# Optimization experiments

Measured on AMD Instinct MI355X. Metric: run time of the kernel, lower is better.

Reference implementation:

```python
import jax, jax.numpy as jnp
import numpy as np

N = 4096   # nodes
E = 65536  # edges
D_IN = 64
H = 128
T = 8
B = 8


def setup_inputs() -> dict:
    key = jax.random.key(0)
    ks = jax.random.split(key, 6)
    x = jax.random.normal(ks[0], (B, T, N, D_IN), jnp.float32)
    edge_index = jax.random.randint(ks[1], (2, E), 0, N, dtype=jnp.int32)
    W0 = jax.random.normal(ks[2], (D_IN + H, 4 * H), jnp.float32) * 0.05
    b0 = jax.random.normal(ks[3], (4 * H,), jnp.float32) * 0.05
    W1 = jax.random.normal(ks[4], (H + H, 4 * H), jnp.float32) * 0.05
    b1 = jax.random.normal(ks[5], (4 * H,), jnp.float32) * 0.05
    return {"x": x, "W0": W0, "b0": b0, "W1": W1, "b1": b1, "edge_index": edge_index}


def _gcn_norm(edge_index, n):
    # PyG GCNConv(improved=True): A_hat = A + 2I, deg over incoming edges (col)
    src, dst = edge_index[0], edge_index[1]
    deg = jax.ops.segment_sum(jnp.ones(edge_index.shape[1], jnp.float32), dst, num_segments=n) + 2.0
    dinv = jax.lax.rsqrt(deg)  # deg >= 2 always, safe
    return src, dst, dinv


def _gcn_gates(comb, W, b, src, dst, dinv, n):
    # comb: (b, n, i+h) -> gates: (b, n, 4h)
    xw = jnp.einsum('bnf,fg->bng', comb, W)
    norm_e = dinv[src] * dinv[dst]                      # (E,)
    msgs = xw[:, src, :] * norm_e[None, :, None]        # (b, E, 4h)
    agg = jax.vmap(lambda m: jax.ops.segment_sum(m, dst, num_segments=n))(msgs)
    # self-loop with weight 2: norm = 2 * dinv[i]^2
    agg = agg + (2.0 * dinv * dinv)[None, :, None] * xw + b
    return agg


def reference(x, W0, b0, W1, b1, edge_index):
    src, dst, dinv = _gcn_norm(edge_index, N)

    def run_layer(seq, W, b):
        h_dim = W.shape[1] // 4

        def step(carry, xt):
            h, c = carry
            comb = jnp.concatenate([xt, h], axis=-1)
            gates = _gcn_gates(comb, W, b, src, dst, dinv, N)
            ci, cf, co, cg = jnp.split(gates, 4, axis=-1)
            i = jax.nn.sigmoid(ci)
            f = jax.nn.sigmoid(cf)
            o = jax.nn.sigmoid(co)
            g = jnp.tanh(cg)
            c_next = f * c + i * g
            h_next = o * jnp.tanh(c_next)
            return (h_next, c_next), h_next

        h0 = jnp.zeros((seq.shape[1], N, h_dim), seq.dtype)
        _, hs = jax.lax.scan(step, (h0, h0), seq)
        return hs  # (t, b, n, h)

    seq = jnp.swapaxes(x, 0, 1)  # batch_first -> (t, b, n, d)
    hs0 = run_layer(seq, W0, b0)
    hs1 = run_layer(hs0, W1, b1)
    return jnp.swapaxes(hs1, 0, 1)  # (b, t, n, h) last-layer output sequence
```

## Files before the change

kernel.cpp:

```cpp
#include <hip/hip_runtime.h>
#include <hip/hip_fp16.h>
#include <math.h>

constexpr int N_NODES = 4096;
constexpr int N_EDGES = 65536;
constexpr int D_INF   = 64;
constexpr int H       = 128;
constexpr int T       = 8;
constexpr int B       = 8;
constexpr int M       = B * N_NODES;

typedef __attribute__((ext_vector_type(8))) short bf16x8;
typedef __attribute__((ext_vector_type(4))) float f32x4;
typedef __attribute__((ext_vector_type(8))) _Float16 f16x8;

__device__ inline unsigned short f2bf(float x) {
  unsigned int u = __float_as_uint(x);
  unsigned int r = (u + 0x7fffu + ((u >> 16) & 1u)) >> 16;
  return (unsigned short)r;
}
__device__ inline float bf2f(unsigned short b) {
  return __uint_as_float((unsigned int)b << 16);
}
__device__ __forceinline__ int swz(int s) { return s ^ (((s >> 7) & 7) << 3); }


__global__ void k_count(const int* __restrict__ dst, int* __restrict__ cnt) {
  int e = blockIdx.x * blockDim.x + threadIdx.x;
  if (e < N_EDGES) atomicAdd(&cnt[dst[e]], 1);
}

__global__ void k_dinv(const int* __restrict__ cnt, float* __restrict__ dinv) {
  int n = blockIdx.x * blockDim.x + threadIdx.x;
  if (n < N_NODES) dinv[n] = 1.0f / sqrtf((float)cnt[n] + 2.0f);
}

__global__ void k_scan(const int* __restrict__ cnt, int* __restrict__ rowptr) {
  __shared__ int sums[1024];
  int t = threadIdx.x;
  int v0 = cnt[4*t+0], v1 = cnt[4*t+1], v2 = cnt[4*t+2], v3 = cnt[4*t+3];
  int s0 = v0, s1 = s0 + v1, s2 = s1 + v2, s3 = s2 + v3;
  sums[t] = s3;
  __syncthreads();
  for (int off = 1; off < 1024; off <<= 1) {
    int x = (t >= off) ? sums[t - off] : 0;
    __syncthreads();
    sums[t] += x;
    __syncthreads();
  }
  int base = (t > 0) ? sums[t - 1] : 0;
  if (t == 0) rowptr[0] = 0;
  rowptr[4*t+1] = base + s0;
  rowptr[4*t+2] = base + s1;
  rowptr[4*t+3] = base + s2;
  rowptr[4*t+4] = base + s3;
}

__global__ void k_fill(const int* __restrict__ src, const int* __restrict__ dst,
                       const float* __restrict__ dinv, const int* __restrict__ rowptr,
                       int* __restrict__ fill, int2* __restrict__ eg) {
  int e = blockIdx.x * blockDim.x + threadIdx.x;
  if (e >= N_EDGES) return;
  int s = src[e], d = dst[e];
  int p = rowptr[d] + atomicAdd(&fill[d], 1);
  eg[p] = make_int2(s, __float_as_int(dinv[s] * dinv[d]));
}

__global__ void k_pack(const float* __restrict__ W, unsigned short* __restrict__ Bp,
                       int K) {
  int tid = blockIdx.x * 256 + threadIdx.x;
  if (tid >= K * 64) return;
  int lane = tid & 63;
  int ntg  = (tid >> 6) & 31;
  int kb   = tid >> 11;
  int gate = ntg & 3, fg = ntg >> 2;
  int corig = gate * 128 + fg * 16 + (lane & 15);
  int k0 = kb * 32 + (lane >> 4) * 8;
  long obase = ((long)(kb * 32 + ntg) * 64 + lane) * 8;
  long plane = (long)K * 512;
  #pragma unroll
  for (int j = 0; j < 8; ++j) {
    float v = W[(long)(k0 + j) * 512 + corig];
    unsigned short h = f2bf(v);
    Bp[obase + j]         = h;
    Bp[plane + obase + j] = f2bf(v - bf2f(h));
  }
}

template<int K, bool L0>
__global__ __launch_bounds__(512, 4) void k_fused(
    const int* __restrict__ rowptr, const int2* __restrict__ eg,
    const float* __restrict__ dinv,
    const float* __restrict__ X32,
    const _Float16* __restrict__ PH0,
    const _Float16* __restrict__ PH1,
    const unsigned short* __restrict__ Bp, const float* __restrict__ bias,
    _Float16* __restrict__ hout, float* __restrict__ cbuf,
    float* __restrict__ out2, int t) {
  constexpr int KB = K / 32;
  __shared__ __align__(16) unsigned short At[8 * KB * 64 * 8];
  int tid  = threadIdx.x;
  int lane = tid & 63;
  int w    = tid >> 6;
  int j    = blockIdx.x;
  int b    = j & 7;
  int n0   = (j >> 3) * 64;
  int m0   = b * N_NODES + n0;
  int g    = lane >> 4, l = lane & 15;
  int c4   = l * 4, c8 = l * 8;

  const float*    Ax   = L0 ? (X32 + (long)b * ((long)T * N_NODES * D_INF)) : nullptr;
  const _Float16* Ah_p = L0 ? nullptr : (PH0 + (long)b * N_NODES * H);
  const _Float16* Bh_p = (L0 ? PH0 : PH1) + (long)b * N_NODES * H;
  constexpr int kbB0 = (L0 ? 64 : 128) >> 5;
  int lane2f = 16 * (l & 3);
  int kbB    = kbB0 + (c8 >> 5);
  int kbA16  = c8 >> 5;
  int kbA32  = c4 >> 5;
  int subA32 = (l & 7) >> 1;
  int j0A32  = (l & 1) * 4;

  #pragma unroll
  for (int nd = 0; nd < 2; ++nd) {
    int r  = (w << 3) + (g << 1) + nd;
    int n  = n0 + r;
    int rs = rowptr[n], re = rowptr[n + 1];
    float accA[8] = {0.f,0.f,0.f,0.f,0.f,0.f,0.f,0.f};
    float accB[8] = {0.f,0.f,0.f,0.f,0.f,0.f,0.f,0.f};
    int e = rs;
    for (; e + 3 < re; e += 4) {
      int2 q0 = eg[e], q1 = eg[e + 1], q2 = eg[e + 2], q3 = eg[e + 3];
      float w0 = __int_as_float(q0.y), w1 = __int_as_float(q1.y);
      float w2 = __int_as_float(q2.y), w3 = __int_as_float(q3.y);
      if constexpr (L0) {
        f32x4 a0 = *(const f32x4*)(Ax + (long)q0.x * D_INF + c4);
        f32x4 a1 = *(const f32x4*)(Ax + (long)q1.x * D_INF + c4);
        f32x4 a2 = *(const f32x4*)(Ax + (long)q2.x * D_INF + c4);
        f32x4 a3 = *(const f32x4*)(Ax + (long)q3.x * D_INF + c4);
        #pragma unroll
        for (int q = 0; q < 4; ++q)
          accA[q] += w0 * a0[q] + w1 * a1[q] + w2 * a2[q] + w3 * a3[q];
      } else {
        f16x8 a0 = *(const f16x8*)(Ah_p + (long)q0.x * H + c8);
        f16x8 a1 = *(const f16x8*)(Ah_p + (long)q1.x * H + c8);
        f16x8 a2 = *(const f16x8*)(Ah_p + (long)q2.x * H + c8);
        f16x8 a3 = *(const f16x8*)(Ah_p + (long)q3.x * H + c8);
        #pragma unroll
        for (int q = 0; q < 8; ++q)
          accA[q] += w0 * (float)a0[q] + w1 * (float)a1[q]
                   + w2 * (float)a2[q] + w3 * (float)a3[q];
      }
      f16x8 b0 = *(const f16x8*)(Bh_p + (long)q0.x * H + c8);
      f16x8 b1 = *(const f16x8*)(Bh_p + (long)q1.x * H + c8);
      f16x8 b2 = *(const f16x8*)(Bh_p + (long)q2.x * H + c8);
      f16x8 b3 = *(const f16x8*)(Bh_p + (long)q3.x * H + c8);
      #pragma unroll
      for (int q = 0; q < 8; ++q)
        accB[q] += w0 * (float)b0[q] + w1 * (float)b1[q]
                 + w2 * (float)b2[q] + w3 * (float)b3[q];
    }
    for (; e < re; ++e) {
      int2 q0 = eg[e];
      float w0 = __int_as_float(q0.y);
      if constexpr (L0) {
        f32x4 a0 = *(const f32x4*)(Ax + (long)q0.x * D_INF + c4);
        #pragma unroll
        for (int q = 0; q < 4; ++q) accA[q] += w0 * a0[q];
      } else {
        f16x8 a0 = *(const f16x8*)(Ah_p + (long)q0.x * H + c8);
        #pragma unroll
        for (int q = 0; q < 8; ++q) accA[q] += w0 * (float)a0[q];
      }
      f16x8 b0 = *(const f16x8*)(Bh_p + (long)q0.x * H + c8);
      #pragma unroll
      for (int q = 0; q < 8; ++q) accB[q] += w0 * (float)b0[q];
    }
    float dn = dinv[n];
    float sw = 2.0f * dn * dn;
    if constexpr (L0) {
      f32x4 a = *(const f32x4*)(Ax + (long)n * D_INF + c4);
      #pragma unroll
      for (int q = 0; q < 4; ++q) accA[q] += sw * a[q];
    } else {
      f16x8 a = *(const f16x8*)(Ah_p + (long)n * H + c8);
      #pragma unroll
      for (int q = 0; q < 8; ++q) accA[q] += sw * (float)a[q];
    }
    {
      f16x8 v = *(const f16x8*)(Bh_p + (long)n * H + c8);
      #pragma unroll
      for (int q = 0; q < 8; ++q) accB[q] += sw * (float)v[q];
    }

    int mt    = r >> 4;
    int lane2 = (r & 15) + lane2f;
    {
      bf16x8 hv, lv;
      #pragma unroll
      for (int q = 0; q < 8; ++q) {
        unsigned short hs = f2bf(accB[q]);
        hv[q] = (short)hs;
        lv[q] = (short)f2bf(accB[q] - bf2f(hs));
      }
      *(bf16x8*)(At + swz((((mt)     * KB + kbB) * 64 + lane2) * 8)) = hv;
      *(bf16x8*)(At + swz((((4 + mt) * KB + kbB) * 64 + lane2) * 8)) = lv;
    }
    if constexpr (L0) {
      unsigned long long hv = 0ull, lv = 0ull;
      #pragma unroll
      for (int q = 0; q < 4; ++q) {
        unsigned short hs = f2bf(accA[q]);
        unsigned short ls = f2bf(accA[q] - bf2f(hs));
        hv |= (unsigned long long)hs << (16 * q);
        lv |= (unsigned long long)ls << (16 * q);
      }
      int lA = (r & 15) + 16 * subA32;
      *(unsigned long long*)(At + swz((((mt)     * KB + kbA32) * 64 + lA) * 8 + j0A32)) = hv;
      *(unsigned long long*)(At + swz((((4 + mt) * KB + kbA32) * 64 + lA) * 8 + j0A32)) = lv;
    } else {
      bf16x8 hv, lv;
      #pragma unroll
      for (int q = 0; q < 8; ++q) {
        unsigned short hs = f2bf(accA[q]);
        hv[q] = (short)hs;
        lv[q] = (short)f2bf(accA[q] - bf2f(hs));
      }
      *(bf16x8*)(At + swz((((mt)     * KB + kbA16) * 64 + lane2) * 8)) = hv;
      *(bf16x8*)(At + swz((((4 + mt) * KB + kbA16) * 64 + lane2) * 8)) = lv;
    }
  }
  __syncthreads();

  int l15 = lane & 15, lq = lane >> 4;
  const unsigned short* bb  = Bp + (long)(w * 4) * 512 + lane * 8;
  const unsigned short* blp = bb + (long)K * 512;

  f32x4 acc[4][4];
  #pragma unroll
  for (int mt = 0; mt < 4; ++mt)
    #pragma unroll
    for (int gt = 0; gt < 4; ++gt)
      acc[mt][gt] = (f32x4){0.f, 0.f, 0.f, 0.f};

  __builtin_amdgcn_s_setprio(1);
  #pragma unroll 2
  for (int kb = 0; kb < KB; ++kb) {
    bf16x8 AH_[4], AL_[4];
    #pragma unroll
    for (int mt = 0; mt < 4; ++mt) {
      AH_[mt] = *(const bf16x8*)(At + swz((((mt)     * KB + kb) * 64 + lane) * 8));
      AL_[mt] = *(const bf16x8*)(At + swz((((4 + mt) * KB + kb) * 64 + lane) * 8));
    }
    bf16x8 BH[4], BL[4];
    #pragma unroll
    for (int gt = 0; gt < 4; ++gt) {
      BH[gt] = *(const bf16x8*)(bb  + ((long)kb * 32 + gt) * 512);
      BL[gt] = *(const bf16x8*)(blp + ((long)kb * 32 + gt) * 512);
    }
    #pragma unroll
    for (int gt = 0; gt < 4; ++gt) {
      #pragma unroll
      for (int mt = 0; mt < 4; ++mt) {
        acc[mt][gt] = __builtin_amdgcn_mfma_f32_16x16x32_bf16(AH_[mt], BH[gt], acc[mt][gt], 0, 0, 0);
        acc[mt][gt] = __builtin_amdgcn_mfma_f32_16x16x32_bf16(AL_[mt], BH[gt], acc[mt][gt], 0, 0, 0);
        acc[mt][gt] = __builtin_amdgcn_mfma_f32_16x16x32_bf16(AH_[mt], BL[gt], acc[mt][gt], 0, 0, 0);
      }
    }
  }
  __builtin_amdgcn_s_setprio(0);

  int f = w * 16 + l15;
  float bi = bias[f], bff = bias[128 + f], bo = bias[256 + f], bg = bias[384 + f];
  #pragma unroll
  for (int mt = 0; mt < 4; ++mt) {
    #pragma unroll
    for (int r = 0; r < 4; ++r) {
      int m = m0 + mt * 16 + lq * 4 + r;
      float vi = 1.0f / (1.0f + __expf(-(acc[mt][0][r] + bi)));
      float vf = 1.0f / (1.0f + __expf(-(acc[mt][1][r] + bff)));
      float vo = 1.0f / (1.0f + __expf(-(acc[mt][2][r] + bo)));
      float vg = tanhf(acc[mt][3][r] + bg);
      long idx = (long)m * H + f;
      float cn = vf * cbuf[idx] + vi * vg;
      float hn = vo * tanhf(cn);
      cbuf[idx] = cn;
      hout[idx] = (_Float16)hn;
      if (out2) {
        int bb2 = m >> 12, nn = m & (N_NODES - 1);
        __builtin_nontemporal_store(hn,
            &out2[(((long)bb2 * T + t) * N_NODES + nn) * H + f]);
      }
    }
  }
}


extern "C" void kernel_launch(void* const* d_in, const int* in_sizes, int n_in,
                              void* d_out, int out_size, void* d_ws, size_t ws_size,
                              hipStream_t stream) {
  const float* x  = (const float*)d_in[0];
  const float* W0 = (const float*)d_in[1];
  const float* b0 = (const float*)d_in[2];
  const float* W1 = (const float*)d_in[3];
  const float* b1 = (const float*)d_in[4];
  const int*   ei = (const int*)d_in[5];
  const int* srcp = ei;
  const int* dstp = ei + N_EDGES;
  float* out = (float*)d_out;

  char* p = (char*)d_ws;
  auto alloc = [&](size_t bytes) {
    char* r = p;
    p += (bytes + 255) & ~(size_t)255;
    return r;
  };
  int*   cnt    = (int*)  alloc(N_NODES * 4);
  int*   fill   = (int*)  alloc(N_NODES * 4);
  float* dinv   = (float*)alloc(N_NODES * 4);
  int*   rowptr = (int*)  alloc((N_NODES + 1) * 4);
  int2*  eg     = (int2*) alloc((size_t)N_EDGES * 8);
  float* cc     = (float*)alloc((size_t)2 * M * H * 4);
  _Float16* hh  = (_Float16*)alloc((size_t)4 * M * H * 2);
  unsigned short* Bp0 = (unsigned short*)alloc((size_t)192 * 512 * 2 * 2);
  unsigned short* Bp1 = (unsigned short*)alloc((size_t)256 * 512 * 2 * 2);
  float*    c0  = cc;
  float*    c1  = cc + (size_t)M * H;
  _Float16* h0a = hh;
  _Float16* h0b = hh + (size_t)M * H;
  _Float16* h1a = hh + (size_t)2 * M * H;
  _Float16* h1b = hh + (size_t)3 * M * H;

  hipMemsetAsync(cnt,  0, N_NODES * 4, stream);
  hipMemsetAsync(fill, 0, N_NODES * 4, stream);
  hipMemsetAsync(cc,   0, (size_t)2 * M * H * 4, stream);
  hipMemsetAsync(hh,   0, (size_t)4 * M * H * 2, stream);

  k_count<<<N_EDGES / 256, 256, 0, stream>>>(dstp, cnt);
  k_dinv <<<N_NODES / 256, 256, 0, stream>>>(cnt, dinv);
  k_scan <<<1, 1024, 0, stream>>>(cnt, rowptr);
  k_fill <<<N_EDGES / 256, 256, 0, stream>>>(srcp, dstp, dinv, rowptr, fill, eg);
  k_pack <<<(192 * 64 + 255) / 256, 256, 0, stream>>>(W0, Bp0, 192);
  k_pack <<<(256 * 64 + 255) / 256, 256, 0, stream>>>(W1, Bp1, 256);

  for (int t = 0; t < T; ++t) {
    const _Float16* h0r = (t & 1) ? h0b : h0a;
    _Float16*       h0w = (t & 1) ? h0a : h0b;
    const _Float16* h1r = (t & 1) ? h1b : h1a;
    _Float16*       h1w = (t & 1) ? h1a : h1b;
    k_fused<192, true><<<512, 512, 0, stream>>>(rowptr, eg, dinv,
        x + (size_t)t * N_NODES * D_INF, h0r, nullptr,
        Bp0, b0, h0w, c0, nullptr, t);
    k_fused<256, false><<<512, 512, 0, stream>>>(rowptr, eg, dinv,
        nullptr, h0w, h1r,
        Bp1, b1, h1w, c1, out, t);
  }
}
```

Baseline: 795.9 us.

## Sort nodes by degree and pair light/heavy nodes for balanced gather

Adds a counting sort of nodes by in-degree and remaps each block's rows so every lane group processes one low-degree and one high-degree node. This evens out the per-wave edge-gather loop length, reducing divergence and tail imbalance in the fused aggregation kernel. Output rows are written through an LDS node map, which makes epilogue stores scattered per row and adds a few small preprocessing kernels.

```diff
diff --git a/kernel.cpp b/kernel.cpp
--- a/kernel.cpp
+++ b/kernel.cpp
@@ -64,6 +64,33 @@
   int s = src[e], d = dst[e];
   int p = rowptr[d] + atomicAdd(&fill[d], 1);
   eg[p] = make_int2(s, __float_as_int(dinv[s] * dinv[d]));
+}
+
+__global__ void k_hist(const int* __restrict__ cnt, int* __restrict__ hist) {
+  int n = blockIdx.x * blockDim.x + threadIdx.x;
+  if (n < N_NODES) atomicAdd(&hist[min(cnt[n], 127)], 1);
+}
+
+__global__ void k_hscan(const int* __restrict__ hist, int* __restrict__ hbase) {
+  __shared__ int sh[128];
+  int t = threadIdx.x;
+  sh[t] = hist[t];
+  __syncthreads();
+  for (int off = 1; off < 128; off <<= 1) {
+    int x = (t >= off) ? sh[t - off] : 0;
+    __syncthreads();
+    sh[t] += x;
+    __syncthreads();
+  }
+  hbase[t] = sh[t] - hist[t];
+}
+
+__global__ void k_place(const int* __restrict__ cnt, const int* __restrict__ hbase,
+                        int* __restrict__ filld, int* __restrict__ sorted) {
+  int n = blockIdx.x * blockDim.x + threadIdx.x;
+  if (n >= N_NODES) return;
+  int d = min(cnt[n], 127);
+  sorted[hbase[d] + atomicAdd(&filld[d], 1)] = n;
 }
 
 __global__ void k_pack(const float* __restrict__ W, unsigned short* __restrict__ Bp,
@@ -90,7 +117,7 @@
 template<int K, bool L0>
 __global__ __launch_bounds__(512, 4) void k_fused(
     const int* __restrict__ rowptr, const int2* __restrict__ eg,
-    const float* __restrict__ dinv,
+    const float* __restrict__ dinv, const int* __restrict__ sorted,
     const float* __restrict__ X32,
     const _Float16* __restrict__ PH0,
     const _Float16* __restrict__ PH1,
@@ -99,13 +126,13 @@
     float* __restrict__ out2, int t) {
   constexpr int KB = K / 32;
   __shared__ __align__(16) unsigned short At[8 * KB * 64 * 8];
+  __shared__ int nodeLDS[64];
   int tid  = threadIdx.x;
   int lane = tid & 63;
   int w    = tid >> 6;
   int j    = blockIdx.x;
   int b    = j & 7;
-  int n0   = (j >> 3) * 64;
-  int m0   = b * N_NODES + n0;
+  int jj   = j >> 3;
   int g    = lane >> 4, l = lane & 15;
   int c4   = l * 4, c8 = l * 8;
 
@@ -123,7 +150,9 @@
   #pragma unroll
   for (int nd = 0; nd < 2; ++nd) {
     int r  = (w << 3) + (g << 1) + nd;
-    int n  = n0 + r;
+    int pairIdx = jj * 32 + (r >> 1);
+    int n  = (r & 1) ? sorted[N_NODES - 1 - pairIdx] : sorted[pairIdx];
+    if (l == 0) nodeLDS[r] = n;
     int rs = rowptr[n], re = rowptr[n + 1];
     float accA[8] = {0.f,0.f,0.f,0.f,0.f,0.f,0.f,0.f};
     float accB[8] = {0.f,0.f,0.f,0.f,0.f,0.f,0.f,0.f};
@@ -275,20 +304,20 @@
   for (int mt = 0; mt < 4; ++mt) {
     #pragma unroll
     for (int r = 0; r < 4; ++r) {
-      int m = m0 + mt * 16 + lq * 4 + r;
+      int rt = mt * 16 + lq * 4 + r;
+      int n2 = nodeLDS[rt];
       float vi = 1.0f / (1.0f + __expf(-(acc[mt][0][r] + bi)));
       float vf = 1.0f / (1.0f + __expf(-(acc[mt][1][r] + bff)));
       float vo = 1.0f / (1.0f + __expf(-(acc[mt][2][r] + bo)));
       float vg = tanhf(acc[mt][3][r] + bg);
-      long idx = (long)m * H + f;
+      long idx = ((long)b * N_NODES + n2) * H + f;
       float cn = vf * cbuf[idx] + vi * vg;
       float hn = vo * tanhf(cn);
       cbuf[idx] = cn;
       hout[idx] = (_Float16)hn;
       if (out2) {
-        int bb2 = m >> 12, nn = m & (N_NODES - 1);
         __builtin_nontemporal_store(hn,
-            &out2[(((long)bb2 * T + t) * N_NODES + nn) * H + f]);
+            &out2[(((long)b * T + t) * N_NODES + n2) * H + f]);
       }
     }
   }
@@ -319,6 +348,10 @@
   float* dinv   = (float*)alloc(N_NODES * 4);
   int*   rowptr = (int*)  alloc((N_NODES + 1) * 4);
   int2*  eg     = (int2*) alloc((size_t)N_EDGES * 8);
+  int*   hist   = (int*)  alloc(128 * 4);
+  int*   hbase  = (int*)  alloc(128 * 4);
+  int*   filld  = (int*)  alloc(128 * 4);
+  int*   sorted = (int*)  alloc(N_NODES * 4);
   float* cc     = (float*)alloc((size_t)2 * M * H * 4);
   _Float16* hh  = (_Float16*)alloc((size_t)4 * M * H * 2);
   unsigned short* Bp0 = (unsigned short*)alloc((size_t)192 * 512 * 2 * 2);
@@ -330,15 +363,20 @@
   _Float16* h1a = hh + (size_t)2 * M * H;
   _Float16* h1b = hh + (size_t)3 * M * H;
 
-  hipMemsetAsync(cnt,  0, N_NODES * 4, stream);
-  hipMemsetAsync(fill, 0, N_NODES * 4, stream);
-  hipMemsetAsync(cc,   0, (size_t)2 * M * H * 4, stream);
-  hipMemsetAsync(hh,   0, (size_t)4 * M * H * 2, stream);
+  hipMemsetAsync(cnt,   0, N_NODES * 4, stream);
+  hipMemsetAsync(fill,  0, N_NODES * 4, stream);
+  hipMemsetAsync(hist,  0, 128 * 4, stream);
+  hipMemsetAsync(filld, 0, 128 * 4, stream);
+  hipMemsetAsync(cc,    0, (size_t)2 * M * H * 4, stream);
+  hipMemsetAsync(hh,    0, (size_t)4 * M * H * 2, stream);
 
   k_count<<<N_EDGES / 256, 256, 0, stream>>>(dstp, cnt);
   k_dinv <<<N_NODES / 256, 256, 0, stream>>>(cnt, dinv);
   k_scan <<<1, 1024, 0, stream>>>(cnt, rowptr);
   k_fill <<<N_EDGES / 256, 256, 0, stream>>>(srcp, dstp, dinv, rowptr, fill, eg);
+  k_hist <<<N_NODES / 256, 256, 0, stream>>>(cnt, hist);
+  k_hscan<<<1, 128, 0, stream>>>(hist, hbase);
+  k_place<<<N_NODES / 256, 256, 0, stream>>>(cnt, hbase, filld, sorted);
   k_pack <<<(192 * 64 + 255) / 256, 256, 0, stream>>>(W0, Bp0, 192);
   k_pack <<<(256 * 64 + 255) / 256, 256, 0, stream>>>(W1, Bp1, 256);
 
@@ -347,10 +385,10 @@
     _Float16*       h0w = (t & 1) ? h0a : h0b;
     const _Float16* h1r = (t & 1) ? h1b : h1a;
     _Float16*       h1w = (t & 1) ? h1a : h1b;
-    k_fused<192, true><<<512, 512, 0, stream>>>(rowptr, eg, dinv,
+    k_fused<192, true><<<512, 512, 0, stream>>>(rowptr, eg, dinv, sorted,
         x + (size_t)t * N_NODES * D_INF, h0r, nullptr,
         Bp0, b0, h0w, c0, nullptr, t);
-    k_fused<256, false><<<512, 512, 0, stream>>>(rowptr, eg, dinv,
+    k_fused<256, false><<<512, 512, 0, stream>>>(rowptr, eg, dinv, sorted,
         nullptr, h0w, h1r,
         Bp1, b1, h1w, c1, out, t);
   }
```

Result: faster. 772.4 us (-3.0%).
